# Kernel optimization log

Hardware: AMD Instinct MI355X
Metric: run time of the kernel (lower is better)

The kernel has to match this reference:

```python
import jax, jax.numpy as jnp
import numpy as np

IN_F, OUT_F = 64, 32
N = IN_F * OUT_F + OUT_F  # 2080 sampled parameters (weights + bias)
B, S = 8, 2048
SCALE_INIT = 1.0 * float(np.sqrt(2.0 / (IN_F + OUT_F)))


def setup_inputs() -> dict:
    key = jax.random.key(0)
    k_x, k_eps, k_loc, k_cov = jax.random.split(key, 4)
    x = jax.random.normal(k_x, (B, S, IN_F), dtype=jnp.float32)
    eps = jax.random.normal(k_eps, (B, S, N), dtype=jnp.float32)
    loc = 0.01 * jax.random.normal(k_loc, (N,), dtype=jnp.float32)
    logvar = jnp.full((N,), float(np.log(SCALE_INIT)), dtype=jnp.float32)
    n_off = N * (N - 1) // 2
    cov_flat = 0.001 * jax.random.normal(k_cov, (n_off,), dtype=jnp.float32)
    return {"x": x, "eps": eps, "loc": loc, "logvar": logvar, "cov_flat": cov_flat}


def reference(x, eps, loc, logvar, cov_flat):
    n = loc.shape[0]
    in_f = x.shape[-1]
    out_f = n // (in_f + 1)  # n = out*(in+1)
    # flat_to_triangular (strictly lower) + make_cholesky, vectorized scatter
    rows, cols = np.tril_indices(n, -1)
    A = jnp.zeros((n, n), dtype=x.dtype).at[rows, cols].set(cov_flat)
    L = A + jnp.diag(jnp.exp(logvar * 0.5))  # off-diag from cov, diag = std
    # MultivariateNormal rsample: loc + L @ eps (per batch sample)
    W = loc + jnp.einsum('bsn,mn->bsm', eps, L)  # [B,S,N]
    b = W[..., :out_f]
    Wm = W[..., out_f:].reshape(*W.shape[:-1], in_f, out_f)  # [B,S,in,out]
    y = jnp.einsum('bsh,bshk->bsk', x, Wm) + b
    return y
```

## Files before the change

### kernel.cpp

```cpp
#include <hip/hip_runtime.h>
#include <hip/hip_bf16.h>

#define IN_F  64
#define OUT_F 32
#define NV    2080
#define NPAD  2176
#define MM    16384
#define KK    2080
#define NBN   17

#define NB_CVT (MM * KK / 8 / 256)
#define NB_L   (NPAD * KK / 256)

typedef __attribute__((ext_vector_type(4))) float f32x4;
typedef __bf16 bf16x8 __attribute__((ext_vector_type(8)));

using gas_ptr = const __attribute__((address_space(1))) void*;
using lds_ptr = __attribute__((address_space(3))) void*;

__global__ __launch_bounds__(256) void prep_k(const float* __restrict__ cov,
                                              const float* __restrict__ logvar,
                                              const float4* __restrict__ eps4,
                                              uint4* __restrict__ epsb,
                                              __hip_bfloat16* __restrict__ LB) {
    if (blockIdx.x < NB_CVT) {
        const size_t i = (size_t)blockIdx.x * 256 + threadIdx.x;
        float4 a = eps4[2 * i];
        float4 b = eps4[2 * i + 1];
        union { uint4 u; __hip_bfloat16 h[8]; } o;
        o.h[0] = __float2bfloat16(a.x); o.h[1] = __float2bfloat16(a.y);
        o.h[2] = __float2bfloat16(a.z); o.h[3] = __float2bfloat16(a.w);
        o.h[4] = __float2bfloat16(b.x); o.h[5] = __float2bfloat16(b.y);
        o.h[6] = __float2bfloat16(b.z); o.h[7] = __float2bfloat16(b.w);
        epsb[i] = o.u;
    } else {
        const int idx = (blockIdx.x - NB_CVT) * 256 + threadIdx.x;
        const int m = idx / KK;
        const int k = idx - m * KK;
        float v = 0.0f;
        if (m < NV) {
            if (k < m)       v = cov[(size_t)(m * (m - 1) / 2) + k];
            else if (k == m) v = expf(0.5f * logvar[m]);
        }
        LB[idx] = __float2bfloat16(v);
    }
}

__global__ __launch_bounds__(256) void gemm_zl_k(const __hip_bfloat16* __restrict__ A,
                                                 const __hip_bfloat16* __restrict__ BT,
                                                 const float* __restrict__ loc,
                                                 const float* __restrict__ x,
                                                 float* __restrict__ Ypart) {
    __shared__ __align__(16) __hip_bfloat16 As[2][128 * 32];
    __shared__ __align__(16) __hip_bfloat16 Bs[2][128 * 32];
    __shared__ float xs[128][4];

    const int tid  = threadIdx.x;
    const int bm   = blockIdx.x;
    const int bn   = (NBN - 1) - blockIdx.y;
    const int wave = tid >> 6;
    const int lane = tid & 63;
    const int quad = lane >> 4;
    const int r16  = lane & 15;

    const int kblocks = min(KK / 32, 4 * bn + 4);

    {
        const int tl = tid >> 1;
        const int cc = (tid & 1) * 2;
#pragma unroll
        for (int c = cc; c < cc + 2; c++) {
            const int h = 4 * bn - 1 + c;
            float w = 0.0f;
            if (bn == 0 && c == 0)          w = 1.0f;
            else if (h >= 0 && h < IN_F)    w = x[(size_t)(bm * 128 + tl) * IN_F + h];
            xs[tl][c] = w;
        }
    }

    const __hip_bfloat16* Ag = A  + (size_t)bm * 128 * KK;
    const __hip_bfloat16* Bg = BT + (size_t)bn * 128 * KK;

    const int c0 = tid, c1 = tid + 256;
    const int ar0 = c0 >> 2, ap0 = (c0 & 3) ^ ((ar0 >> 1) & 3);
    const int ar1 = c1 >> 2, ap1 = (c1 & 3) ^ ((ar1 >> 1) & 3);
    const size_t gofs0 = (size_t)ar0 * KK + ap0 * 8;
    const size_t gofs1 = (size_t)ar1 * KK + ap1 * 8;

    f32x4 acc[2][8];
#pragma unroll
    for (int i = 0; i < 2; i++)
#pragma unroll
        for (int j = 0; j < 8; j++) acc[i][j] = f32x4{0.f, 0.f, 0.f, 0.f};

    int aofs[2], bofs[8];
#pragma unroll
    for (int i = 0; i < 2; i++) {
        const int arow = 32 * wave + 16 * i + r16;
        aofs[i] = arow * 32 + (quad ^ ((arow >> 1) & 3)) * 8;
    }
#pragma unroll
    for (int j = 0; j < 8; j++) {
        const int brow = 16 * j + r16;
        bofs[j] = brow * 32 + (quad ^ ((brow >> 1) & 3)) * 8;
    }

    __builtin_amdgcn_global_load_lds((gas_ptr)(Ag + gofs0), (lds_ptr)(&As[0][0] + c0 * 8), 16, 0, 0);
    __builtin_amdgcn_global_load_lds((gas_ptr)(Ag + gofs1), (lds_ptr)(&As[0][0] + c1 * 8), 16, 0, 0);
    __builtin_amdgcn_global_load_lds((gas_ptr)(Bg + gofs0), (lds_ptr)(&Bs[0][0] + c0 * 8), 16, 0, 0);
    __builtin_amdgcn_global_load_lds((gas_ptr)(Bg + gofs1), (lds_ptr)(&Bs[0][0] + c1 * 8), 16, 0, 0);

    for (int kb = 0; kb < kblocks; ++kb) {
        const int cur = kb & 1;
        __syncthreads();

        if (kb + 1 < kblocks) {
            const size_t k0 = (size_t)(kb + 1) * 32;
            __builtin_amdgcn_global_load_lds((gas_ptr)(Ag + k0 + gofs0), (lds_ptr)(&As[cur ^ 1][0] + c0 * 8), 16, 0, 0);
            __builtin_amdgcn_global_load_lds((gas_ptr)(Ag + k0 + gofs1), (lds_ptr)(&As[cur ^ 1][0] + c1 * 8), 16, 0, 0);
            __builtin_amdgcn_global_load_lds((gas_ptr)(Bg + k0 + gofs0), (lds_ptr)(&Bs[cur ^ 1][0] + c0 * 8), 16, 0, 0);
            __builtin_amdgcn_global_load_lds((gas_ptr)(Bg + k0 + gofs1), (lds_ptr)(&Bs[cur ^ 1][0] + c1 * 8), 16, 0, 0);
        }

        bf16x8 af[2], bfr[8];
#pragma unroll
        for (int i = 0; i < 2; i++) af[i]  = *(const bf16x8*)(&As[cur][0] + aofs[i]);
#pragma unroll
        for (int j = 0; j < 8; j++) bfr[j] = *(const bf16x8*)(&Bs[cur][0] + bofs[j]);
#pragma unroll
        for (int i = 0; i < 2; i++)
#pragma unroll
            for (int j = 0; j < 8; j++)
                acc[i][j] = __builtin_amdgcn_mfma_f32_16x16x32_bf16(af[i], bfr[j], acc[i][j], 0, 0, 0);
    }

    float locv[8];
#pragma unroll
    for (int j = 0; j < 8; j++) {
        const int col = bn * 128 + 16 * j + r16;
        locv[j] = (col < NV) ? loc[col] : 0.0f;
    }

    float* yp = Ypart + ((size_t)bn * MM + (size_t)bm * 128) * OUT_F;
#pragma unroll
    for (int i = 0; i < 2; i++) {
#pragma unroll
        for (int r = 0; r < 4; r++) {
            const int tl = 32 * wave + 16 * i + 4 * quad + r;
            float v0 = 0.0f, v1 = 0.0f;
#pragma unroll
            for (int c = 0; c < 4; c++) {
                const float w = xs[tl][c];
                v0 += w * (acc[i][2 * c][r]     + locv[2 * c]);
                v1 += w * (acc[i][2 * c + 1][r] + locv[2 * c + 1]);
            }
            yp[(size_t)tl * OUT_F + r16]      = v0;
            yp[(size_t)tl * OUT_F + 16 + r16] = v1;
        }
    }
}

__global__ __launch_bounds__(256) void reduce_y_k(const float4* __restrict__ yp,
                                                  float4* __restrict__ y) {
    const size_t i = (size_t)blockIdx.x * 256 + threadIdx.x;
    float4 s = yp[i];
#pragma unroll
    for (int b = 1; b < NBN; b++) {
        float4 v = yp[i + (size_t)b * (MM * OUT_F / 4)];
        s.x += v.x; s.y += v.y; s.z += v.z; s.w += v.w;
    }
    y[i] = s;
}

extern "C" void kernel_launch(void* const* d_in, const int* in_sizes, int n_in,
                              void* d_out, int out_size, void* d_ws, size_t ws_size,
                              hipStream_t stream) {
    const float* x      = (const float*)d_in[0];
    const float* eps    = (const float*)d_in[1];
    const float* loc    = (const float*)d_in[2];
    const float* logvar = (const float*)d_in[3];
    const float* cov    = (const float*)d_in[4];
    float* y = (float*)d_out;

    char* ws = (char*)d_ws;
    __hip_bfloat16* EpsB  = (__hip_bfloat16*)ws;
    __hip_bfloat16* LB    = (__hip_bfloat16*)(ws + (size_t)MM * KK * 2);
    float*          Ypart = (float*)(ws + (size_t)MM * KK * 2
                                        + (size_t)NPAD * KK * 2);

    prep_k<<<NB_CVT + NB_L, 256, 0, stream>>>(cov, logvar, (const float4*)eps,
                                              (uint4*)EpsB, LB);
    gemm_zl_k<<<dim3(MM / 128, NBN), 256, 0, stream>>>(EpsB, LB, loc, x, Ypart);
    reduce_y_k<<<(MM * OUT_F / 4) / 256, 256, 0, stream>>>((const float4*)Ypart, (float4*)y);
}
```

Baseline: 323.1 us.

## Fuse eps fp32-to-bf16 conversion into GEMM A-tile loads

Removes the separate pass that converted eps to bf16 in workspace; the GEMM now loads fp32 eps directly into registers, converts to bf16 and stores to LDS after the MFMAs of each k-step. This avoids writing and re-reading a large bf16 copy of eps. In exchange, each GEMM block reads fp32 eps (twice the bytes per tile), and eps tiles are re-read by each of the up-to-17 column blocks. The A path also moves from direct global-to-LDS loads to register staging, which adds register pressure.

```diff
diff --git a/kernel.cpp b/kernel.cpp
--- a/kernel.cpp
+++ b/kernel.cpp
@@ -9,44 +9,27 @@
 #define KK    2080
 #define NBN   17
 
-#define NB_CVT (MM * KK / 8 / 256)
-#define NB_L   (NPAD * KK / 256)
-
 typedef __attribute__((ext_vector_type(4))) float f32x4;
 typedef __bf16 bf16x8 __attribute__((ext_vector_type(8)));
 
 using gas_ptr = const __attribute__((address_space(1))) void*;
 using lds_ptr = __attribute__((address_space(3))) void*;
 
-__global__ __launch_bounds__(256) void prep_k(const float* __restrict__ cov,
-                                              const float* __restrict__ logvar,
-                                              const float4* __restrict__ eps4,
-                                              uint4* __restrict__ epsb,
-                                              __hip_bfloat16* __restrict__ LB) {
-    if (blockIdx.x < NB_CVT) {
-        const size_t i = (size_t)blockIdx.x * 256 + threadIdx.x;
-        float4 a = eps4[2 * i];
-        float4 b = eps4[2 * i + 1];
-        union { uint4 u; __hip_bfloat16 h[8]; } o;
-        o.h[0] = __float2bfloat16(a.x); o.h[1] = __float2bfloat16(a.y);
-        o.h[2] = __float2bfloat16(a.z); o.h[3] = __float2bfloat16(a.w);
-        o.h[4] = __float2bfloat16(b.x); o.h[5] = __float2bfloat16(b.y);
-        o.h[6] = __float2bfloat16(b.z); o.h[7] = __float2bfloat16(b.w);
-        epsb[i] = o.u;
-    } else {
-        const int idx = (blockIdx.x - NB_CVT) * 256 + threadIdx.x;
-        const int m = idx / KK;
-        const int k = idx - m * KK;
-        float v = 0.0f;
-        if (m < NV) {
-            if (k < m)       v = cov[(size_t)(m * (m - 1) / 2) + k];
-            else if (k == m) v = expf(0.5f * logvar[m]);
-        }
-        LB[idx] = __float2bfloat16(v);
-    }
-}
-
-__global__ __launch_bounds__(256) void gemm_zl_k(const __hip_bfloat16* __restrict__ A,
+__global__ __launch_bounds__(256) void build_L_k(const float* __restrict__ cov,
+                                                 const float* __restrict__ logvar,
+                                                 __hip_bfloat16* __restrict__ LB) {
+    const int idx = blockIdx.x * 256 + threadIdx.x;
+    const int m = idx / KK;
+    const int k = idx - m * KK;
+    float v = 0.0f;
+    if (m < NV) {
+        if (k < m)       v = cov[(size_t)(m * (m - 1) / 2) + k];
+        else if (k == m) v = expf(0.5f * logvar[m]);
+    }
+    LB[idx] = __float2bfloat16(v);
+}
+
+__global__ __launch_bounds__(256) void gemm_zl_k(const float* __restrict__ A,
                                                  const __hip_bfloat16* __restrict__ BT,
                                                  const float* __restrict__ loc,
                                                  const float* __restrict__ x,
@@ -78,7 +61,7 @@
         }
     }
 
-    const __hip_bfloat16* Ag = A  + (size_t)bm * 128 * KK;
+    const float*          Ag = A  + (size_t)bm * 128 * KK;
     const __hip_bfloat16* Bg = BT + (size_t)bn * 128 * KK;
 
     const int c0 = tid, c1 = tid + 256;
@@ -105,19 +88,35 @@
         bofs[j] = brow * 32 + (quad ^ ((brow >> 1) & 3)) * 8;
     }
 
-    __builtin_amdgcn_global_load_lds((gas_ptr)(Ag + gofs0), (lds_ptr)(&As[0][0] + c0 * 8), 16, 0, 0);
-    __builtin_amdgcn_global_load_lds((gas_ptr)(Ag + gofs1), (lds_ptr)(&As[0][0] + c1 * 8), 16, 0, 0);
-    __builtin_amdgcn_global_load_lds((gas_ptr)(Bg + gofs0), (lds_ptr)(&Bs[0][0] + c0 * 8), 16, 0, 0);
-    __builtin_amdgcn_global_load_lds((gas_ptr)(Bg + gofs1), (lds_ptr)(&Bs[0][0] + c1 * 8), 16, 0, 0);
+    {
+        f32x4 ra0 = *(const f32x4*)(Ag + gofs0);
+        f32x4 ra1 = *(const f32x4*)(Ag + gofs0 + 4);
+        f32x4 ra2 = *(const f32x4*)(Ag + gofs1);
+        f32x4 ra3 = *(const f32x4*)(Ag + gofs1 + 4);
+        __builtin_amdgcn_global_load_lds((gas_ptr)(Bg + gofs0), (lds_ptr)(&Bs[0][0] + c0 * 8), 16, 0, 0);
+        __builtin_amdgcn_global_load_lds((gas_ptr)(Bg + gofs1), (lds_ptr)(&Bs[0][0] + c1 * 8), 16, 0, 0);
+        bf16x8 w0, w1;
+#pragma unroll
+        for (int q = 0; q < 4; q++) {
+            w0[q] = (__bf16)ra0[q]; w0[4 + q] = (__bf16)ra1[q];
+            w1[q] = (__bf16)ra2[q]; w1[4 + q] = (__bf16)ra3[q];
+        }
+        *(bf16x8*)(&As[0][0] + c0 * 8) = w0;
+        *(bf16x8*)(&As[0][0] + c1 * 8) = w1;
+    }
 
     for (int kb = 0; kb < kblocks; ++kb) {
         const int cur = kb & 1;
         __syncthreads();
 
-        if (kb + 1 < kblocks) {
+        const bool pf = (kb + 1 < kblocks);
+        f32x4 ra0, ra1, ra2, ra3;
+        if (pf) {
             const size_t k0 = (size_t)(kb + 1) * 32;
-            __builtin_amdgcn_global_load_lds((gas_ptr)(Ag + k0 + gofs0), (lds_ptr)(&As[cur ^ 1][0] + c0 * 8), 16, 0, 0);
-            __builtin_amdgcn_global_load_lds((gas_ptr)(Ag + k0 + gofs1), (lds_ptr)(&As[cur ^ 1][0] + c1 * 8), 16, 0, 0);
+            ra0 = *(const f32x4*)(Ag + k0 + gofs0);
+            ra1 = *(const f32x4*)(Ag + k0 + gofs0 + 4);
+            ra2 = *(const f32x4*)(Ag + k0 + gofs1);
+            ra3 = *(const f32x4*)(Ag + k0 + gofs1 + 4);
             __builtin_amdgcn_global_load_lds((gas_ptr)(Bg + k0 + gofs0), (lds_ptr)(&Bs[cur ^ 1][0] + c0 * 8), 16, 0, 0);
             __builtin_amdgcn_global_load_lds((gas_ptr)(Bg + k0 + gofs1), (lds_ptr)(&Bs[cur ^ 1][0] + c1 * 8), 16, 0, 0);
         }
@@ -132,6 +131,17 @@
 #pragma unroll
             for (int j = 0; j < 8; j++)
                 acc[i][j] = __builtin_amdgcn_mfma_f32_16x16x32_bf16(af[i], bfr[j], acc[i][j], 0, 0, 0);
+
+        if (pf) {
+            bf16x8 w0, w1;
+#pragma unroll
+            for (int q = 0; q < 4; q++) {
+                w0[q] = (__bf16)ra0[q]; w0[4 + q] = (__bf16)ra1[q];
+                w1[q] = (__bf16)ra2[q]; w1[4 + q] = (__bf16)ra3[q];
+            }
+            *(bf16x8*)(&As[cur ^ 1][0] + c0 * 8) = w0;
+            *(bf16x8*)(&As[cur ^ 1][0] + c1 * 8) = w1;
+        }
     }
 
     float locv[8];
@@ -183,13 +193,10 @@
     float* y = (float*)d_out;
 
     char* ws = (char*)d_ws;
-    __hip_bfloat16* EpsB  = (__hip_bfloat16*)ws;
-    __hip_bfloat16* LB    = (__hip_bfloat16*)(ws + (size_t)MM * KK * 2);
-    float*          Ypart = (float*)(ws + (size_t)MM * KK * 2
-                                        + (size_t)NPAD * KK * 2);
-
-    prep_k<<<NB_CVT + NB_L, 256, 0, stream>>>(cov, logvar, (const float4*)eps,
-                                              (uint4*)EpsB, LB);
-    gemm_zl_k<<<dim3(MM / 128, NBN), 256, 0, stream>>>(EpsB, LB, loc, x, Ypart);
+    __hip_bfloat16* LB    = (__hip_bfloat16*)ws;
+    float*          Ypart = (float*)(ws + (size_t)NPAD * KK * 2);
+
+    build_L_k<<<(NPAD * KK) / 256, 256, 0, stream>>>(cov, logvar, LB);
+    gemm_zl_k<<<dim3(MM / 128, NBN), 256, 0, stream>>>(eps, LB, loc, x, Ypart);
     reduce_y_k<<<(MM * OUT_F / 4) / 256, 256, 0, stream>>>((const float4*)Ypart, (float4*)y);
 }
```

Result: faster. 316.0 us (-2.2%).
